# Performance work log

Measured on AMD Instinct MI355X. Metric: run time of the kernel, lower is better.

Reference implementation:

```python
import jax, jax.numpy as jnp
from jax import lax
import numpy as np

# (cin, cout, kernel, pad) for the 18 convs (funs 1,3,5,6,7,9,10,11,13..17,19..23)
CONVS = [(3,32,3,0),(32,64,3,0),(64,128,3,1),(128,64,1,0),(64,128,3,1),
         (128,256,3,1),(256,128,1,0),(128,256,3,0),(256,512,3,1),(512,256,1,0),
         (256,512,3,1),(512,256,1,0),(256,512,3,0),(512,256,3,1),(256,128,1,0),
         (128,64,3,1),(64,32,1,0),(32,6,3,1)]
# maxpool(2,2) after conv index (1-based) -> pool padding (torch pads with -inf, floor mode)
POOL_AFTER = {1: 1, 2: 1, 5: 0, 8: 1, 13: 1}
GT = (0.567, 0.469, 0.206, 0.53)  # hardcoded ground-truth box (cx, cy, w, h), normalized


def _backbone(x, ws, bs):
    for i, (w, b) in enumerate(zip(ws, bs), 1):
        pad = CONVS[i - 1][3]
        x = lax.conv_general_dilated(
            x, w, (1, 1), [(pad, pad), (pad, pad)],
            dimension_numbers=("NCHW", "OIHW", "NCHW")) + b[None, :, None, None]
        if i in POOL_AFTER:
            p = POOL_AFTER[i]
            x = lax.reduce_window(
                x, -jnp.inf, lax.max, (1, 1, 2, 2), (1, 1, 2, 2),
                [(0, 0), (0, 0), (p, p), (p, p)])
    return x


def _head(x):
    # torch: x.transpose(1,3) on [B,6,H,W] -> [B,W,H,6]; j indexes W, k indexes H
    xt = jnp.transpose(x, (0, 3, 2, 1))
    B, W, H, _ = xt.shape
    j = jnp.arange(W, dtype=xt.dtype)[None, :, None]  # [1,W,1]
    k = jnp.arange(H, dtype=xt.dtype)[None, None, :]  # [1,1,H]
    px = (j + xt[..., 2]) / W
    py = (k + xt[..., 3]) / H
    pw = jnp.exp(xt[..., 4]) / W
    ph = jnp.exp(xt[..., 5]) / H
    # center-format IoU against the single gt box (detached mask, as in torch via float())
    iw = jnp.clip(jnp.minimum(px + pw * 0.5, GT[0] + GT[2] * 0.5)
                  - jnp.maximum(px - pw * 0.5, GT[0] - GT[2] * 0.5), 0.0)
    ih = jnp.clip(jnp.minimum(py + ph * 0.5, GT[1] + GT[3] * 0.5)
                  - jnp.maximum(py - ph * 0.5, GT[1] - GT[3] * 0.5), 0.0)
    inter = iw * ih
    iou = inter / (pw * ph + GT[2] * GT[3] - inter)
    iou = lax.stop_gradient(iou)
    tx = GT[0] * W - j          # [1,W,1]
    ty = GT[1] * H - k          # [1,1,H]
    tw = np.log(GT[2] * W).astype(np.float32)
    th = np.log(GT[3] * H).astype(np.float32)
    l1 = (jnp.abs(tx - xt[..., 2]) + jnp.abs(ty - xt[..., 3])
          + jnp.abs(tw - xt[..., 4]) + jnp.abs(th - xt[..., 5]))
    loss = jnp.sum(jnp.where(iou > 0.5, l1, 0.0)).reshape(1)
    return xt, loss


def setup_inputs() -> dict:
    key = jax.random.key(0)
    keys = jax.random.split(key, 1 + 2 * len(CONVS))
    d = {"x": jax.random.normal(keys[0], (16, 3, 416, 416), jnp.float32)}
    for i, (cin, cout, ks, _) in enumerate(CONVS, 1):
        fan_in = cin * ks * ks
        d[f"w{i}"] = jax.random.normal(keys[2 * i - 1], (cout, cin, ks, ks), jnp.float32) / np.sqrt(fan_in)
        d[f"b{i}"] = jax.random.normal(keys[2 * i], (cout,), jnp.float32) * 0.01
    return d


def reference(x, w1, b1, w2, b2, w3, b3, w4, b4, w5, b5, w6, b6, w7, b7, w8, b8,
              w9, b9, w10, b10, w11, b11, w12, b12, w13, b13, w14, b14, w15, b15,
              w16, b16, w17, b17, w18, b18):
    ws = [w1, w2, w3, w4, w5, w6, w7, w8, w9, w10, w11, w12, w13, w14, w15, w16, w17, w18]
    bs = [b1, b2, b3, b4, b5, b6, b7, b8, b9, b10, b11, b12, b13, b14, b15, b16, b17, b18]
    feat = _backbone(x, ws, bs)
    xt, loss = _head(feat)
    return (xt, loss)
```

## Files before the change

### kernel.cpp

```cpp
#include <hip/hip_runtime.h>
#include <math.h>

typedef short v8s __attribute__((ext_vector_type(8)));
typedef float v4f __attribute__((ext_vector_type(4)));

template<int K, int COT, bool POOL, bool MASK, bool SWAP>
__global__ __launch_bounds__(256) void conv_fused(
    const float* __restrict__ in, const float* __restrict__ wgt,
    const float* __restrict__ bias, float* __restrict__ out,
    int B, int Cin, int Hin, int Win,
    int Hc, int Wc, int Hout, int Wout,
    int Cout, int cpad, int ppad,
    int inPS, int inRS, int inOfs, int outPS, int outRS, int outOfs)
{
    constexpr int NPY = POOL ? 2 : 1;
    constexpr int PS  = K + NPY - 1;
    const int spatial = Hout * Wout;
    const int idx = (SWAP ? blockIdx.y : blockIdx.x) * blockDim.x + threadIdx.x;
    const int cog = SWAP ? blockIdx.x : blockIdx.y;
    const int total = B * spatial;
    if (idx >= total) return;
    const int b  = idx / spatial;
    const int sp = idx - b * spatial;
    const int oy = sp / Wout;
    const int ox = sp - oy * Wout;
    const int co0 = cog * COT;

    const int cy0 = POOL ? (2 * oy - ppad) : oy;
    const int cx0 = POOL ? (2 * ox - ppad) : ox;
    const int iy0 = cy0 - cpad;
    const int ix0 = cx0 - cpad;

    bool my[PS], mx[PS];
#pragma unroll
    for (int i = 0; i < PS; i++) {
        my[i] = !MASK || ((unsigned)(iy0 + i) < (unsigned)Hin);
        mx[i] = !MASK || ((unsigned)(ix0 + i) < (unsigned)Win);
    }

    float acc[COT][NPY * NPY];
#pragma unroll
    for (int c = 0; c < COT; c++)
#pragma unroll
        for (int p = 0; p < NPY * NPY; p++) acc[c][p] = 0.f;

    const float* inB = in + inOfs + (size_t)b * Cin * inPS;
    const long wBase  = (long)co0 * Cin * K * K;

    for (int ci = 0; ci < Cin; ci++) {
        const float* ip = inB + (size_t)ci * inPS;
        float patch[PS][PS];
#pragma unroll
        for (int py = 0; py < PS; py++) {
#pragma unroll
            for (int px = 0; px < PS; px++) {
                float v = 0.f;
                if (my[py] && mx[px]) v = ip[(iy0 + py) * inRS + (ix0 + px)];
                patch[py][px] = v;
            }
        }
        const float* wp = wgt + wBase + (long)ci * K * K;
#pragma unroll
        for (int c = 0; c < COT; c++) {
#pragma unroll
            for (int kh = 0; kh < K; kh++)
#pragma unroll
            for (int kw = 0; kw < K; kw++) {
                const float wv = wp[(long)c * Cin * K * K + kh * K + kw];
#pragma unroll
                for (int dy = 0; dy < NPY; dy++)
#pragma unroll
                for (int dx = 0; dx < NPY; dx++)
                    acc[c][dy * NPY + dx] = fmaf(wv, patch[dy + kh][dx + kw],
                                                 acc[c][dy * NPY + dx]);
            }
        }
    }

#pragma unroll
    for (int c = 0; c < COT; c++) {
        float v;
        if (POOL) {
            v = -INFINITY;
#pragma unroll
            for (int dy = 0; dy < NPY; dy++)
#pragma unroll
            for (int dx = 0; dx < NPY; dx++) {
                const int cy = cy0 + dy, cx = cx0 + dx;
                if ((unsigned)cy < (unsigned)Hc && (unsigned)cx < (unsigned)Wc)
                    v = fmaxf(v, acc[c][dy * NPY + dx]);
            }
        } else {
            v = acc[c][0];
        }
        v += bias[co0 + c];
        out[outOfs + (size_t)(b * Cout + co0 + c) * outPS + oy * outRS + ox] = v;
    }
}

__global__ __launch_bounds__(256) void ring_zero(
    float* __restrict__ buf, int planes, int H, int W)
{
    int Wp = W + 2, Hp = H + 2;
    int ringlen = 2 * Wp + 2 * H;
    int t = blockIdx.x * 256 + threadIdx.x;
    if (t >= planes * ringlen) return;
    int p = t / ringlen, r = t - p * ringlen;
    float* pl = buf + (size_t)p * Hp * Wp;
    int idx;
    if (r < Wp) idx = r;
    else if (r < 2 * Wp) idx = (Hp - 1) * Wp + (r - Wp);
    else { int rr = r - 2 * Wp; int row = 1 + (rr >> 1); idx = row * Wp + ((rr & 1) ? (Wp - 1) : 0); }
    pl[idx] = 0.f;
}

__device__ __forceinline__ unsigned short f2bf_rne(float x) {
    unsigned u = __float_as_uint(x);
    return (unsigned short)((u + 0x7fffu + ((u >> 16) & 1u)) >> 16);
}
__device__ __forceinline__ float bf2f(unsigned short h) {
    return __uint_as_float(((unsigned)h) << 16);
}

__global__ __launch_bounds__(256) void prepack(
    const float* __restrict__ w, unsigned short* __restrict__ hi,
    unsigned short* __restrict__ lo, int cout, int kdim, int nkb)
{
    int t = blockIdx.x * 256 + threadIdx.x;
    if (t >= cout * kdim) return;
    int co = t / kdim, k = t - co * kdim;
    int cb = co >> 4, m = co & 15, kb = k >> 5, kk = k & 31;
    int lane = ((kk >> 3) << 4) | m, j = kk & 7;
    long dst = ((long)(cb * nkb + kb) << 9) + lane * 8 + j;
    float x = w[t];
    unsigned short h = f2bf_rne(x);
    hi[dst] = h;
    lo[dst] = f2bf_rne(x - bf2f(h));
}

template<int MT, int KS, bool SPLIT>
__global__ __launch_bounds__(256) void conv_mfma(
    const float* __restrict__ in, const unsigned short* __restrict__ whi,
    const unsigned short* __restrict__ wlo, const float* __restrict__ bias,
    float* __restrict__ out, int Cin, int inHWp, int inWp, int Hc, int Wc,
    int Cout, int pad, int b0, int nb, int nkbTot, int nkbPer, int Mpad,
    int outHWp, int outWp)
{
    const int HW = Hc * Wc;
    const int M = nb * HW;
    const int tid = threadIdx.x;
    const int lane = tid & 63;
    const int wv = tid >> 6;
    const int spBase = blockIdx.x * 64;
    const int kb0 = SPLIT ? blockIdx.z * nkbPer : 0;
    const int kb1 = SPLIT ? kb0 + nkbPer : nkbTot;

    __shared__ unsigned short P[2][5120];

    const int spoL = lane >> 2;
    int kkc[2];
    kkc[0] = (tid & 3) + 4 * wv;
    kkc[1] = kkc[0] + 16;

    const float* sptr[4];
    int soff[4];
#pragma unroll
    for (int j = 0; j < 4; ++j) {
        int sp = spBase + spoL + 16 * j;
        int q = sp < M ? sp : M - 1;
        int b = q / HW; int r = q - b * HW;
        int soy = r / Wc, sox = r - soy * Wc;
        soff[j] = (soy + 1) * inWp + (sox + 1);
        sptr[j] = in + (size_t)(b0 + b) * Cin * inHWp;
    }

    int ci[2], r9[2], koff[2];
#pragma unroll
    for (int m = 0; m < 2; ++m) {
        int k = kb0 * 32 + kkc[m];
        if (KS == 3) {
            ci[m] = k / 9; r9[m] = k - 9 * ci[m];
            int d3 = (r9[m] >= 3) + (r9[m] >= 6);
            koff[m] = ci[m] * inHWp + (d3 - pad) * inWp + (r9[m] - 3 * d3 - pad);
        } else { ci[m] = k; koff[m] = k * inHWp; }
    }

    float rv[8];
#define STAGE()                                                                \
    {                                                                          \
        _Pragma("unroll")                                                      \
        for (int m = 0; m < 2; ++m)                                            \
        _Pragma("unroll")                                                      \
        for (int j = 0; j < 4; ++j)                                            \
            rv[m * 4 + j] = sptr[j][koff[m] + soff[j]];                        \
    }
#define ADVANCE()                                                              \
    {                                                                          \
        _Pragma("unroll")                                                      \
        for (int m = 0; m < 2; ++m) {                                          \
            if (KS == 3) {                                                     \
                r9[m] += 5; int c = r9[m] >= 9; r9[m] -= c ? 9 : 0;            \
                ci[m] += 3 + c;                                                \
                int d3 = (r9[m] >= 3) + (r9[m] >= 6);                          \
                koff[m] = ci[m] * inHWp + (d3 - pad) * inWp                    \
                        + (r9[m] - 3 * d3 - pad);                              \
            } else { koff[m] += 32 * inHWp; }                                  \
        }                                                                      \
    }

    STAGE();

    const int g0 = blockIdx.y * (MT * 4) + wv * MT;
    const unsigned short* whp[MT];
    const unsigned short* wlp[MT];
#pragma unroll
    for (int mt = 0; mt < MT; ++mt) {
        size_t base = (((size_t)(g0 + mt) * nkbTot + kb0) << 9) + lane * 8;
        whp[mt] = whi + base; wlp[mt] = wlo + base;
    }

    v4f acc[MT][4];
    {
        v4f z = {0.f, 0.f, 0.f, 0.f};
#pragma unroll
        for (int mt = 0; mt < MT; ++mt)
#pragma unroll
            for (int nt = 0; nt < 4; ++nt) acc[mt][nt] = z;
    }

    for (int kb = kb0; kb < kb1; ++kb) {
        unsigned short* Ph = P[kb & 1];
#pragma unroll
        for (int m = 0; m < 2; ++m)
#pragma unroll
        for (int j = 0; j < 4; ++j) {
            float v = rv[m * 4 + j];
            unsigned vb = __float_as_uint(v);
            float res = v - __uint_as_float(vb & 0xffff0000u);
            int a = (spoL + 16 * j) * 40 + kkc[m];
            Ph[a] = (unsigned short)(vb >> 16);
            Ph[2560 + a] = (unsigned short)(__float_as_uint(res) >> 16);
        }
        __syncthreads();

        v8s wh[MT], wl[MT];
#pragma unroll
        for (int mt = 0; mt < MT; ++mt) {
            wh[mt] = *(const v8s*)whp[mt];
            wl[mt] = *(const v8s*)wlp[mt];
            whp[mt] += 512; wlp[mt] += 512;
        }

        if (kb + 1 < kb1) { ADVANCE(); STAGE(); }

#pragma unroll
        for (int nt = 0; nt < 4; ++nt) {
            int ro = (nt * 16 + (lane & 15)) * 40 + (lane >> 4) * 8;
            v8s ph = *(const v8s*)(Ph + ro);
            v8s pl = *(const v8s*)(Ph + 2560 + ro);
#pragma unroll
            for (int mt = 0; mt < MT; ++mt) {
                acc[mt][nt] = __builtin_amdgcn_mfma_f32_16x16x32_bf16(wh[mt], ph, acc[mt][nt], 0, 0, 0);
                acc[mt][nt] = __builtin_amdgcn_mfma_f32_16x16x32_bf16(wh[mt], pl, acc[mt][nt], 0, 0, 0);
                acc[mt][nt] = __builtin_amdgcn_mfma_f32_16x16x32_bf16(wl[mt], ph, acc[mt][nt], 0, 0, 0);
            }
        }
    }
#undef STAGE
#undef ADVANCE

    const int qrow = (lane >> 4) * 4;
    if (SPLIT) {
        float* pz = out + (size_t)blockIdx.z * Cout * Mpad;
#pragma unroll
        for (int mt = 0; mt < MT; ++mt) {
            int co = (g0 + mt) * 16 + qrow;
#pragma unroll
            for (int nt = 0; nt < 4; ++nt) {
                int sp = spBase + nt * 16 + (lane & 15);
                if (sp < M) {
#pragma unroll
                    for (int r = 0; r < 4; ++r)
                        pz[(size_t)(co + r) * Mpad + sp] = acc[mt][nt][r];
                }
            }
        }
    } else {
#pragma unroll
        for (int mt = 0; mt < MT; ++mt) {
            int co = (g0 + mt) * 16 + qrow;
            float bsv[4];
#pragma unroll
            for (int r = 0; r < 4; ++r) bsv[r] = bias[co + r];
#pragma unroll
            for (int nt = 0; nt < 4; ++nt) {
                int sp = spBase + nt * 16 + (lane & 15);
                if (sp < M) {
                    int b = sp / HW, rsp = sp - b * HW;
                    int y = rsp / Wc, xx = rsp - y * Wc;
                    float* op = out + (size_t)(b * Cout + co) * outHWp
                              + (size_t)(y + 1) * outWp + (xx + 1);
#pragma unroll
                    for (int r = 0; r < 4; ++r)
                        op[(size_t)r * outHWp] = acc[mt][nt][r] + bsv[r];
                }
            }
        }
    }
}

__global__ __launch_bounds__(256) void sk_reduce(
    const float* __restrict__ part, const float* __restrict__ bias,
    float* __restrict__ out, int Cout, int HW, int Wc, int M, int Mpad, int SK,
    int outHWp, int outWp)
{
    int t = blockIdx.x * 256 + threadIdx.x;
    if (t >= Cout * M) return;
    int co = t / M, m = t - co * M;
    float s = bias[co];
    for (int k = 0; k < SK; ++k)
        s += part[((size_t)k * Cout + co) * Mpad + m];
    int b = m / HW, rsp = m - b * HW;
    int y = rsp / Wc, xx = rsp - y * Wc;
    out[(size_t)(b * Cout + co) * outHWp + (size_t)(y + 1) * outWp + (xx + 1)] = s;
}

__global__ __launch_bounds__(256) void maxpool_k(
    const float* __restrict__ in, float* __restrict__ out,
    int Hc, int Wc, int Hp, int Wp, int p, int total,
    int inHWp, int inWp, int outHWp, int outWp)
{
    int t = blockIdx.x * 256 + threadIdx.x;
    if (t >= total) return;
    int wp2 = Hp * Wp;
    int bc = t / wp2; int r = t - bc * wp2;
    int y = r / Wp, xx = r - y * Wp;
    int y0 = 2 * y - p, x0 = 2 * xx - p;
    const float* ip = in + (size_t)bc * inHWp;
    float v = -INFINITY;
#pragma unroll
    for (int dy = 0; dy < 2; ++dy)
#pragma unroll
    for (int dx = 0; dx < 2; ++dx) {
        int yy = y0 + dy, xc = x0 + dx;
        if ((unsigned)yy < (unsigned)Hc && (unsigned)xc < (unsigned)Wc)
            v = fmaxf(v, ip[(yy + 1) * inWp + (xc + 1)]);
    }
    out[(size_t)bc * outHWp + (size_t)(y + 1) * outWp + (xx + 1)] = v;
}

__global__ __launch_bounds__(1024) void head_kernel(
    const float* __restrict__ x, float* __restrict__ out, int B)
{
    const int W = 13, H = 13;
    const float gx = 0.567f, gy = 0.469f, gw = 0.206f, gh = 0.53f;
    const int tid = threadIdx.x;
    const int total = B * W * H;
    float lsum = 0.f;
    for (int i = tid; i < total; i += blockDim.x) {
        const int b = i / (W * H);
        const int r = i - b * W * H;
        const int j = r / H;
        const int k = r - j * H;
        float v[6];
#pragma unroll
        for (int c = 0; c < 6; c++) {
            v[c] = x[((b * 6 + c) * H + k) * W + j];
            out[((b * W + j) * H + k) * 6 + c] = v[c];
        }
        const float px = (j + v[2]) / (float)W;
        const float py = (k + v[3]) / (float)H;
        const float pw = expf(v[4]) / (float)W;
        const float ph = expf(v[5]) / (float)H;
        float iw = fminf(px + pw * 0.5f, gx + gw * 0.5f)
                 - fmaxf(px - pw * 0.5f, gx - gw * 0.5f);
        iw = fmaxf(iw, 0.f);
        float ih = fminf(py + ph * 0.5f, gy + gh * 0.5f)
                 - fmaxf(py - ph * 0.5f, gy - gh * 0.5f);
        ih = fmaxf(ih, 0.f);
        const float inter = iw * ih;
        const float iou = inter / (pw * ph + gw * gh - inter);
        const float tx = gx * W - (float)j;
        const float ty = gy * H - (float)k;
        const float tw = logf(gw * W);
        const float th = logf(gh * H);
        const float l1 = fabsf(tx - v[2]) + fabsf(ty - v[3])
                       + fabsf(tw - v[4]) + fabsf(th - v[5]);
        if (iou > 0.5f) lsum += l1;
    }
    __shared__ float red[1024];
    red[tid] = lsum;
    __syncthreads();
    for (int s = blockDim.x / 2; s > 0; s >>= 1) {
        if (tid < s) red[tid] += red[tid + s];
        __syncthreads();
    }
    if (tid == 0) out[total * 6] = red[0];
}

extern "C" void kernel_launch(void* const* d_in, const int* in_sizes, int n_in,
                              void* d_out, int out_size, void* d_ws, size_t ws_size,
                              hipStream_t stream)
{
    (void)in_sizes; (void)n_in; (void)out_size;
    const float* x = (const float*)d_in[0];
    const int B = 16;
    const size_t MB = 1024 * 1024;
    char* ws = (char*)d_ws;
    float* bufA = (float*)ws;
    float* bufB = (float*)(ws + 93 * MB);
    unsigned short* WHI = (unsigned short*)(ws + 141 * MB);
    unsigned short* WLO = (unsigned short*)(ws + 153 * MB);
    char* TEMP = ws + 165 * MB;
    const bool gemmOK = ws_size >= 166 * MB;
    const size_t tempAvail = ws_size > 165 * MB ? ws_size - 165 * MB : 0;

    static const struct { int cin, cout, ks, cpad, pool, ppad; } L[18] = {
        {3,  32, 3, 0, 1, 1}, {32, 64, 3, 0, 1, 1}, {64, 128, 3, 1, 0, 0},
        {128, 64, 1, 0, 0, 0}, {64, 128, 3, 1, 1, 0}, {128, 256, 3, 1, 0, 0},
        {256, 128, 1, 0, 0, 0}, {128, 256, 3, 0, 1, 1}, {256, 512, 3, 1, 0, 0},
        {512, 256, 1, 0, 0, 0}, {256, 512, 3, 1, 0, 0}, {512, 256, 1, 0, 0, 0},
        {256, 512, 3, 0, 1, 1}, {512, 256, 3, 1, 0, 0}, {256, 128, 1, 0, 0, 0},
        {128, 64, 3, 1, 0, 0}, {64, 32, 1, 0, 0, 0}, {32, 6, 3, 1, 0, 0}
    };
    static const bool RING[18] = {0,1,0,1,1,0,0,1,0,1,0,0,1,0,1,0,1,0};

    if (gemmOK) {
        size_t off = 0;
        for (int i = 1; i <= 15; ++i) {
            int kdim = L[i].cin * L[i].ks * L[i].ks;
            int n = L[i].cout * kdim;
            prepack<<<(n + 255) / 256, 256, 0, stream>>>(
                (const float*)d_in[2 * i + 1], WHI + off, WLO + off,
                L[i].cout, kdim, kdim / 32);
            off += (size_t)n;
        }
    }

    const float* cur = x;
    int Hin = 416, Win = 416;
    size_t woff = 0;

    for (int i = 0; i < 18; ++i) {
        const auto& l = L[i];
        const int Hc = Hin + 2 * l.cpad - l.ks + 1;
        const int Wc = Win + 2 * l.cpad - l.ks + 1;
        const int Hout = l.pool ? (Hc + 2 * l.ppad - 2) / 2 + 1 : Hc;
        const int Wout = l.pool ? (Wc + 2 * l.ppad - 2) / 2 + 1 : Wc;
        float* dst = (i % 2 == 0) ? bufA : bufB;
        const float* w  = (const float*)d_in[2 * i + 1];
        const float* bb = (const float*)d_in[2 * i + 2];
        const int kdim = l.cin * l.ks * l.ks;
        const int nkb = kdim / 32;

        const int inRS  = (i == 0) ? Win : (Win + 2);
        const int inPS  = (i == 0) ? Hin * Win : (Hin + 2) * (Win + 2);
        const int inOfs = (i == 0) ? 0 : (inRS + 1);
        const bool outPad = (i != 17);
        const int outRS  = outPad ? (Wout + 2) : Wout;
        const int outPS  = outPad ? (Hout + 2) * (Wout + 2) : Hout * Wout;
        const int outOfs = outPad ? (outRS + 1) : 0;
        const int tRS = Wc + 2, tPS = (Hc + 2) * (Wc + 2);

        if (RING[i]) {
            int planes = B * l.cout;
            int ringlen = 2 * (Wout + 2) + 2 * Hout;
            ring_zero<<<(planes * ringlen + 255) / 256, 256, 0, stream>>>(
                dst, planes, Hout, Wout);
        }

        int nb = 16;
        if (l.pool) {
            size_t perImg = (size_t)l.cout * tPS * 4;
            while (nb && perImg * (size_t)nb > tempAvail) nb >>= 1;
        }
        const bool useG = gemmOK && i >= 1 && i <= 15 && (!l.pool || nb >= 1);

        if (useG) {
            for (int b0 = 0; b0 < B; b0 += nb) {
                const int M = nb * Hc * Wc;
                const int gx = (M + 63) / 64;
                int MTv = (l.cout >= 256 && (long)gx * (l.cout / 256) >= 512) ? 4
                        : (l.cout >= 128 && (long)gx * (l.cout / 128) >= 512) ? 2 : 1;
                int gy = l.cout / (MTv * 64);
                int SK = 1;
                if (!l.pool && (long)gx * gy < 512) {
                    if (nkb % 4 == 0 && (size_t)4 * l.cout * gx * 64 * 4 <= tempAvail) SK = 4;
                    else if (nkb % 2 == 0 && (size_t)2 * l.cout * gx * 64 * 4 <= tempAvail) SK = 2;
                }
                const int nkbPer = nkb / SK;
                const int Mpad = gx * 64;
                float* gout = l.pool ? (float*)TEMP : (SK > 1 ? (float*)TEMP : dst);
                const int gHWp = l.pool ? tPS : (SK > 1 ? 0 : outPS);
                const int gWp  = l.pool ? tRS : (SK > 1 ? 0 : outRS);
                dim3 gr(gx, gy, SK);
#define GL(MTC, KSC, SPL)                                                      \
                conv_mfma<MTC, KSC, SPL><<<gr, 256, 0, stream>>>(              \
                    cur, WHI + woff, WLO + woff, bb, gout, l.cin, inPS, inRS,  \
                    Hc, Wc, l.cout, l.cpad, b0, nb, nkb, nkbPer, Mpad,         \
                    gHWp, gWp)
#define G2(MTC, KSC) do { if (SK > 1) GL(MTC, KSC, true); else GL(MTC, KSC, false); } while (0)
                if (MTv == 4)      { if (l.ks == 3) G2(4, 3); else G2(4, 1); }
                else if (MTv == 2) { if (l.ks == 3) G2(2, 3); else G2(2, 1); }
                else               { if (l.ks == 3) G2(1, 3); else G2(1, 1); }
#undef G2
#undef GL
                if (SK > 1) {
                    int tot = l.cout * M;
                    sk_reduce<<<(tot + 255) / 256, 256, 0, stream>>>(
                        (const float*)TEMP, bb, dst, l.cout, Hc * Wc, Wc, M,
                        Mpad, SK, outPS, outRS);
                }
                if (l.pool) {
                    int total = nb * l.cout * Hout * Wout;
                    maxpool_k<<<(total + 255) / 256, 256, 0, stream>>>(
                        (const float*)TEMP,
                        dst + (size_t)b0 * l.cout * outPS,
                        Hc, Wc, Hout, Wout, l.ppad, total, tPS, tRS, outPS, outRS);
                }
            }
        } else {
            const int spatial = Hout * Wout;
#define FL(KK, CC, PP, MM, SW)                                                 \
            conv_fused<KK, CC, PP, MM, SW><<<                                  \
                SW ? dim3(l.cout / CC, (B * spatial + 255) / 256)              \
                   : dim3((B * spatial + 255) / 256, l.cout / CC),             \
                256, 0, stream>>>(                                             \
                cur, w, bb, dst, B, l.cin, Hin, Win, Hc, Wc, Hout, Wout,       \
                l.cout, l.cpad, l.ppad, inPS, inRS, inOfs, outPS, outRS, outOfs)
            if (i == 0)                           FL(3, 8, true, true, true);
            else if (i == 16)                     FL(1, 8, false, false, false);
            else if (i == 17)                     FL(3, 6, false, false, false);
            else if (l.pool)                      FL(3, 4, true, true, false);
            else if (l.ks == 3)                   FL(3, 8, false, true, false);
            else                                  FL(1, 8, false, true, false);
#undef FL
        }

        if (i >= 1 && i <= 15) woff += (size_t)l.cout * kdim;
        cur = dst;
        Hin = Hout;
        Win = Wout;
    }

    head_kernel<<<1, 1024, 0, stream>>>(cur, (float*)d_out, B);
}
```

Baseline: 1.520 ms.

## Switch activations to padded NHWC and vectorize MFMA conv staging, add 128-wide tile kernel

Moves intermediate activations from padded NCHW planes to a padded NHWC (channel-last) layout. The MFMA implicit-GEMM kernel can then load four consecutive input channels as one v4f and pack bf16 hi/lo pairs into LDS with vector stores. It also adds a double-buffered register prefetch, a 128-row spatial tile variant for layers with 128 or fewer output channels, and a revised split-K/MT selection heuristic. The goal is to cut scattered scalar global loads and LDS stores in the GEMM staging and raise occupancy and reuse. The cost is rewritten ring-zero, prepack, maxpool and reduce indexing, plus more register pressure.

```diff
diff --git a/kernel.cpp b/kernel.cpp
--- a/kernel.cpp
+++ b/kernel.cpp
@@ -3,6 +3,7 @@
 
 typedef short v8s __attribute__((ext_vector_type(8)));
 typedef float v4f __attribute__((ext_vector_type(4)));
+typedef unsigned uu2 __attribute__((ext_vector_type(2)));
 
 template<int K, int COT, bool POOL, bool MASK, bool SWAP>
 __global__ __launch_bounds__(256) void conv_fused(
@@ -11,7 +12,8 @@
     int B, int Cin, int Hin, int Win,
     int Hc, int Wc, int Hout, int Wout,
     int Cout, int cpad, int ppad,
-    int inPS, int inRS, int inOfs, int outPS, int outRS, int outOfs)
+    long inBS, long inCS, int inRS, int inXS, long inOfs,
+    long outBS, long outCS, int outRS, int outXS, long outOfs)
 {
     constexpr int NPY = POOL ? 2 : 1;
     constexpr int PS  = K + NPY - 1;
@@ -44,18 +46,19 @@
 #pragma unroll
         for (int p = 0; p < NPY * NPY; p++) acc[c][p] = 0.f;
 
-    const float* inB = in + inOfs + (size_t)b * Cin * inPS;
-    const long wBase  = (long)co0 * Cin * K * K;
+    const float* inB = in + inOfs + (size_t)b * inBS;
+    const long wBase = (long)co0 * Cin * K * K;
 
     for (int ci = 0; ci < Cin; ci++) {
-        const float* ip = inB + (size_t)ci * inPS;
+        const float* ip = inB + (size_t)ci * inCS;
         float patch[PS][PS];
 #pragma unroll
         for (int py = 0; py < PS; py++) {
 #pragma unroll
             for (int px = 0; px < PS; px++) {
                 float v = 0.f;
-                if (my[py] && mx[px]) v = ip[(iy0 + py) * inRS + (ix0 + px)];
+                if (my[py] && mx[px])
+                    v = ip[(iy0 + py) * inRS + (ix0 + px) * inXS];
                 patch[py][px] = v;
             }
         }
@@ -94,24 +97,33 @@
             v = acc[c][0];
         }
         v += bias[co0 + c];
-        out[outOfs + (size_t)(b * Cout + co0 + c) * outPS + oy * outRS + ox] = v;
+        out[outOfs + (size_t)b * outBS + (size_t)(co0 + c) * outCS
+            + oy * outRS + ox * outXS] = v;
     }
 }
 
 __global__ __launch_bounds__(256) void ring_zero(
-    float* __restrict__ buf, int planes, int H, int W)
+    float* __restrict__ buf, int B, int H, int W, int C4)
 {
     int Wp = W + 2, Hp = H + 2;
-    int ringlen = 2 * Wp + 2 * H;
+    int rl4 = (2 * Wp + 2 * H) * C4;
     int t = blockIdx.x * 256 + threadIdx.x;
-    if (t >= planes * ringlen) return;
-    int p = t / ringlen, r = t - p * ringlen;
-    float* pl = buf + (size_t)p * Hp * Wp;
-    int idx;
-    if (r < Wp) idx = r;
-    else if (r < 2 * Wp) idx = (Hp - 1) * Wp + (r - Wp);
-    else { int rr = r - 2 * Wp; int row = 1 + (rr >> 1); idx = row * Wp + ((rr & 1) ? (Wp - 1) : 0); }
-    pl[idx] = 0.f;
+    if (t >= B * rl4) return;
+    int p = t / rl4, r = t - p * rl4;
+    int top = Wp * C4;
+    int idx4;
+    if (r < top) idx4 = r;
+    else if (r < 2 * top) idx4 = (Hp - 1) * Wp * C4 + (r - top);
+    else {
+        r -= 2 * top;
+        int row = 1 + r / (2 * C4);
+        int rr = r - (row - 1) * (2 * C4);
+        int side = rr / C4;
+        int cc = rr - side * C4;
+        idx4 = (row * Wp + side * (Wp - 1)) * C4 + cc;
+    }
+    v4f z = {0.f, 0.f, 0.f, 0.f};
+    ((v4f*)buf)[(size_t)p * Hp * Wp * C4 + idx4] = z;
 }
 
 __device__ __forceinline__ unsigned short f2bf_rne(float x) {
@@ -124,11 +136,14 @@
 
 __global__ __launch_bounds__(256) void prepack(
     const float* __restrict__ w, unsigned short* __restrict__ hi,
-    unsigned short* __restrict__ lo, int cout, int kdim, int nkb)
-{
+    unsigned short* __restrict__ lo, int cout, int cin, int ksq, int nkb)
+{
+    int kdim = cin * ksq;
     int t = blockIdx.x * 256 + threadIdx.x;
     if (t >= cout * kdim) return;
-    int co = t / kdim, k = t - co * kdim;
+    int co = t / kdim, rem = t - co * kdim;
+    int ci = rem / ksq, off = rem - ci * ksq;
+    int k = off * cin + ci;
     int cb = co >> 4, m = co & 15, kb = k >> 5, kk = k & 31;
     int lane = ((kk >> 3) << 4) | m, j = kk & 7;
     long dst = ((long)(cb * nkb + kb) << 9) + lane * 8 + j;
@@ -138,13 +153,31 @@
     lo[dst] = f2bf_rne(x - bf2f(h));
 }
 
+#define PACK_LDSW(PL, V, ROW, KQ)                                              \
+    {                                                                          \
+        unsigned a0 = __float_as_uint((V)[0]), a1 = __float_as_uint((V)[1]);   \
+        unsigned a2 = __float_as_uint((V)[2]), a3 = __float_as_uint((V)[3]);   \
+        float r0 = (V)[0] - __uint_as_float(a0 & 0xffff0000u);                 \
+        float r1 = (V)[1] - __uint_as_float(a1 & 0xffff0000u);                 \
+        float r2 = (V)[2] - __uint_as_float(a2 & 0xffff0000u);                 \
+        float r3 = (V)[3] - __uint_as_float(a3 & 0xffff0000u);                 \
+        uu2 hp, lp;                                                            \
+        hp[0] = (a0 >> 16) | (a1 & 0xffff0000u);                               \
+        hp[1] = (a2 >> 16) | (a3 & 0xffff0000u);                               \
+        lp[0] = (__float_as_uint(r0) >> 16) | (__float_as_uint(r1) & 0xffff0000u); \
+        lp[1] = (__float_as_uint(r2) >> 16) | (__float_as_uint(r3) & 0xffff0000u); \
+        int a_ = (ROW) * 40 + 4 * (KQ);                                        \
+        *(uu2*)((PL) + a_) = hp;                                               \
+        *(uu2*)((PL) + (LOHALF) + a_) = lp;                                    \
+    }
+
 template<int MT, int KS, bool SPLIT>
 __global__ __launch_bounds__(256) void conv_mfma(
     const float* __restrict__ in, const unsigned short* __restrict__ whi,
     const unsigned short* __restrict__ wlo, const float* __restrict__ bias,
-    float* __restrict__ out, int Cin, int inHWp, int inWp, int Hc, int Wc,
-    int Cout, int pad, int b0, int nb, int nkbTot, int nkbPer, int Mpad,
-    int outHWp, int outWp)
+    float* __restrict__ out, int Cin, int inBS, int inRow, int Hc, int Wc,
+    int Cout, int pad, int b0, int nb, int nkbTot, int nkbPer,
+    int Mpad, int outBS, int outRow)
 {
     const int HW = Hc * Wc;
     const int M = nb * HW;
@@ -153,62 +186,51 @@
     const int wv = tid >> 6;
     const int spBase = blockIdx.x * 64;
     const int kb0 = SPLIT ? blockIdx.z * nkbPer : 0;
-    const int kb1 = SPLIT ? kb0 + nkbPer : nkbTot;
-
+    const int n = SPLIT ? nkbPer : nkbTot;
+
+#define LOHALF 2560
     __shared__ unsigned short P[2][5120];
 
-    const int spoL = lane >> 2;
-    int kkc[2];
-    kkc[0] = (tid & 3) + 4 * wv;
-    kkc[1] = kkc[0] + 16;
-
-    const float* sptr[4];
-    int soff[4];
-#pragma unroll
-    for (int j = 0; j < 4; ++j) {
-        int sp = spBase + spoL + 16 * j;
+    const int spo = tid >> 3;
+    const int kq  = tid & 7;
+
+    int jbase[2];
+#pragma unroll
+    for (int j = 0; j < 2; ++j) {
+        int sp = spBase + spo + 32 * j;
         int q = sp < M ? sp : M - 1;
         int b = q / HW; int r = q - b * HW;
-        int soy = r / Wc, sox = r - soy * Wc;
-        soff[j] = (soy + 1) * inWp + (sox + 1);
-        sptr[j] = in + (size_t)(b0 + b) * Cin * inHWp;
-    }
-
-    int ci[2], r9[2], koff[2];
-#pragma unroll
-    for (int m = 0; m < 2; ++m) {
-        int k = kb0 * 32 + kkc[m];
+        int y = r / Wc, x = r - y * Wc;
+        jbase[j] = (b0 + b) * inBS + (y + 1) * inRow + (x + 1) * Cin;
+    }
+
+    int koff, rowrem = 0, rowChunks = 0;
+    {
+        int k0 = kb0 * 32;
         if (KS == 3) {
-            ci[m] = k / 9; r9[m] = k - 9 * ci[m];
-            int d3 = (r9[m] >= 3) + (r9[m] >= 6);
-            koff[m] = ci[m] * inHWp + (d3 - pad) * inWp + (r9[m] - 3 * d3 - pad);
-        } else { ci[m] = k; koff[m] = k * inHWp; }
-    }
-
-    float rv[8];
-#define STAGE()                                                                \
+            int off0 = k0 / Cin;
+            int ci0 = k0 - off0 * Cin;
+            int dy0 = off0 / 3, dx0 = off0 - 3 * dy0;
+            int cinCh = Cin >> 5;
+            rowChunks = 3 * cinCh;
+            rowrem = rowChunks - (dx0 * cinCh + (ci0 >> 5));
+            koff = (dy0 - pad) * inRow + (dx0 - pad) * Cin + ci0 + 4 * kq;
+        } else {
+            koff = k0 + 4 * kq;
+        }
+    }
+
+#define STAGE(F)                                                               \
     {                                                                          \
-        _Pragma("unroll")                                                      \
-        for (int m = 0; m < 2; ++m)                                            \
-        _Pragma("unroll")                                                      \
-        for (int j = 0; j < 4; ++j)                                            \
-            rv[m * 4 + j] = sptr[j][koff[m] + soff[j]];                        \
-    }
-#define ADVANCE()                                                              \
+        F[0] = *(const v4f*)(in + jbase[0] + koff);                            \
+        F[1] = *(const v4f*)(in + jbase[1] + koff);                            \
+    }
+#define ADV()                                                                  \
     {                                                                          \
-        _Pragma("unroll")                                                      \
-        for (int m = 0; m < 2; ++m) {                                          \
-            if (KS == 3) {                                                     \
-                r9[m] += 5; int c = r9[m] >= 9; r9[m] -= c ? 9 : 0;            \
-                ci[m] += 3 + c;                                                \
-                int d3 = (r9[m] >= 3) + (r9[m] >= 6);                          \
-                koff[m] = ci[m] * inHWp + (d3 - pad) * inWp                    \
-                        + (r9[m] - 3 * d3 - pad);                              \
-            } else { koff[m] += 32 * inHWp; }                                  \
-        }                                                                      \
-    }
-
-    STAGE();
+        if (KS == 3 && --rowrem == 0) {                                        \
+            rowrem = rowChunks; koff += inRow - 3 * Cin + 32;                  \
+        } else koff += 32;                                                     \
+    }
 
     const int g0 = blockIdx.y * (MT * 4) + wv * MT;
     const unsigned short* whp[MT];
@@ -228,36 +250,175 @@
             for (int nt = 0; nt < 4; ++nt) acc[mt][nt] = z;
     }
 
-    for (int kb = kb0; kb < kb1; ++kb) {
-        unsigned short* Ph = P[kb & 1];
-#pragma unroll
-        for (int m = 0; m < 2; ++m)
-#pragma unroll
-        for (int j = 0; j < 4; ++j) {
-            float v = rv[m * 4 + j];
-            unsigned vb = __float_as_uint(v);
-            float res = v - __uint_as_float(vb & 0xffff0000u);
-            int a = (spoL + 16 * j) * 40 + kkc[m];
-            Ph[a] = (unsigned short)(vb >> 16);
-            Ph[2560 + a] = (unsigned short)(__float_as_uint(res) >> 16);
-        }
+    v4f rv0[2], rv1[2];
+    STAGE(rv0); ADV();
+    if (n > 1) { STAGE(rv1); }
+    ADV();
+
+#define BODY(RV)                                                               \
+    {                                                                          \
+        unsigned short* Pl = &P[cc & 1][0];                                    \
+        PACK_LDSW(Pl, RV[0], spo, kq);                                         \
+        PACK_LDSW(Pl, RV[1], spo + 32, kq);                                    \
+        __syncthreads();                                                       \
+        v8s wh[MT], wl[MT];                                                    \
+        _Pragma("unroll")                                                      \
+        for (int mt = 0; mt < MT; ++mt) {                                      \
+            wh[mt] = *(const v8s*)whp[mt]; whp[mt] += 512;                     \
+            wl[mt] = *(const v8s*)wlp[mt]; wlp[mt] += 512;                     \
+        }                                                                      \
+        if (cc + 2 < n) { STAGE(RV); ADV(); }                                  \
+        _Pragma("unroll")                                                      \
+        for (int nt = 0; nt < 4; ++nt) {                                       \
+            int ro = (nt * 16 + (lane & 15)) * 40 + (lane >> 4) * 8;           \
+            v8s ph = *(const v8s*)(Pl + ro);                                   \
+            v8s pl = *(const v8s*)(Pl + LOHALF + ro);                          \
+            _Pragma("unroll")                                                  \
+            for (int mt = 0; mt < MT; ++mt) {                                  \
+                acc[mt][nt] = __builtin_amdgcn_mfma_f32_16x16x32_bf16(         \
+                    wh[mt], ph, acc[mt][nt], 0, 0, 0);                         \
+                acc[mt][nt] = __builtin_amdgcn_mfma_f32_16x16x32_bf16(         \
+                    wh[mt], pl, acc[mt][nt], 0, 0, 0);                         \
+                acc[mt][nt] = __builtin_amdgcn_mfma_f32_16x16x32_bf16(         \
+                    wl[mt], ph, acc[mt][nt], 0, 0, 0);                         \
+            }                                                                  \
+        }                                                                      \
+    }
+
+    int cc = 0;
+    for (;;) {
+        BODY(rv0);
+        if (++cc >= n) break;
+        BODY(rv1);
+        if (++cc >= n) break;
+    }
+#undef BODY
+#undef STAGE
+#undef ADV
+#undef LOHALF
+
+    const int qrow = (lane >> 4) * 4;
+    if (SPLIT) {
+        float* pz = out + (size_t)blockIdx.z * Mpad * Cout;
+#pragma unroll
+        for (int mt = 0; mt < MT; ++mt) {
+            int co = (g0 + mt) * 16 + qrow;
+#pragma unroll
+            for (int nt = 0; nt < 4; ++nt) {
+                int sp = spBase + nt * 16 + (lane & 15);
+                if (sp < M)
+                    *(v4f*)(pz + (size_t)sp * Cout + co) = acc[mt][nt];
+            }
+        }
+    } else {
+#pragma unroll
+        for (int mt = 0; mt < MT; ++mt) {
+            int co = (g0 + mt) * 16 + qrow;
+            v4f bs = *(const v4f*)(bias + co);
+#pragma unroll
+            for (int nt = 0; nt < 4; ++nt) {
+                int sp = spBase + nt * 16 + (lane & 15);
+                if (sp < M) {
+                    int b = sp / HW, rsp = sp - b * HW;
+                    int y = rsp / Wc, x = rsp - y * Wc;
+                    v4f o = acc[mt][nt] + bs;
+                    *(v4f*)(out + (size_t)b * outBS + (y + 1) * outRow
+                            + (x + 1) * Cout + co) = o;
+                }
+            }
+        }
+    }
+}
+
+template<int MT, int KS>
+__global__ __launch_bounds__(256) void conv_mfma_n128(
+    const float* __restrict__ in, const unsigned short* __restrict__ whi,
+    const unsigned short* __restrict__ wlo, const float* __restrict__ bias,
+    float* __restrict__ out, int Cin, int inBS, int inRow, int Hc, int Wc,
+    int Cout, int pad, int b0, int nb, int nkbTot, int outBS, int outRow)
+{
+    const int HW = Hc * Wc;
+    const int M = nb * HW;
+    const int tid = threadIdx.x;
+    const int lane = tid & 63;
+    const int wv = tid >> 6;
+    const int spBase = blockIdx.x * 128;
+
+#define LOHALF 5120
+    __shared__ unsigned short P[10240];
+
+    const int spo = tid >> 3;
+    const int kq  = tid & 7;
+
+    int jbase[4];
+#pragma unroll
+    for (int j = 0; j < 4; ++j) {
+        int sp = spBase + spo + 32 * j;
+        int q = sp < M ? sp : M - 1;
+        int b = q / HW; int r = q - b * HW;
+        int y = r / Wc, x = r - y * Wc;
+        jbase[j] = (b0 + b) * inBS + (y + 1) * inRow + (x + 1) * Cin;
+    }
+
+    int koff, rowrem = 0, rowChunks = 0;
+    if (KS == 3) {
+        int cinCh = Cin >> 5;
+        rowChunks = 3 * cinCh;
+        rowrem = rowChunks;
+        koff = (0 - pad) * inRow + (0 - pad) * Cin + 4 * kq;
+    } else {
+        koff = 4 * kq;
+    }
+
+    v4f rv[4];
+#pragma unroll
+    for (int j = 0; j < 4; ++j) rv[j] = *(const v4f*)(in + jbase[j] + koff);
+
+    const int g0 = blockIdx.y * (MT * 4) + wv * MT;
+    const unsigned short* whp[MT];
+    const unsigned short* wlp[MT];
+#pragma unroll
+    for (int mt = 0; mt < MT; ++mt) {
+        size_t base = ((size_t)(g0 + mt) * nkbTot << 9) + lane * 8;
+        whp[mt] = whi + base; wlp[mt] = wlo + base;
+    }
+
+    v4f acc[MT][8];
+    {
+        v4f z = {0.f, 0.f, 0.f, 0.f};
+#pragma unroll
+        for (int mt = 0; mt < MT; ++mt)
+#pragma unroll
+            for (int nt = 0; nt < 8; ++nt) acc[mt][nt] = z;
+    }
+
+    for (int cc = 0; cc < nkbTot; ++cc) {
+#pragma unroll
+        for (int j = 0; j < 4; ++j)
+            PACK_LDSW(P, rv[j], spo + 32 * j, kq);
         __syncthreads();
 
         v8s wh[MT], wl[MT];
 #pragma unroll
         for (int mt = 0; mt < MT; ++mt) {
-            wh[mt] = *(const v8s*)whp[mt];
-            wl[mt] = *(const v8s*)wlp[mt];
-            whp[mt] += 512; wlp[mt] += 512;
-        }
-
-        if (kb + 1 < kb1) { ADVANCE(); STAGE(); }
-
-#pragma unroll
-        for (int nt = 0; nt < 4; ++nt) {
+            wh[mt] = *(const v8s*)whp[mt]; whp[mt] += 512;
+            wl[mt] = *(const v8s*)wlp[mt]; wlp[mt] += 512;
+        }
+
+        if (cc + 1 < nkbTot) {
+            if (KS == 3 && --rowrem == 0) {
+                rowrem = rowChunks; koff += inRow - 3 * Cin + 32;
+            } else koff += 32;
+#pragma unroll
+            for (int j = 0; j < 4; ++j)
+                rv[j] = *(const v4f*)(in + jbase[j] + koff);
+        }
+
+#pragma unroll
+        for (int nt = 0; nt < 8; ++nt) {
             int ro = (nt * 16 + (lane & 15)) * 40 + (lane >> 4) * 8;
-            v8s ph = *(const v8s*)(Ph + ro);
-            v8s pl = *(const v8s*)(Ph + 2560 + ro);
+            v8s ph = *(const v8s*)(P + ro);
+            v8s pl = *(const v8s*)(P + LOHALF + ro);
 #pragma unroll
             for (int mt = 0; mt < MT; ++mt) {
                 acc[mt][nt] = __builtin_amdgcn_mfma_f32_16x16x32_bf16(wh[mt], ph, acc[mt][nt], 0, 0, 0);
@@ -265,45 +426,24 @@
                 acc[mt][nt] = __builtin_amdgcn_mfma_f32_16x16x32_bf16(wl[mt], ph, acc[mt][nt], 0, 0, 0);
             }
         }
-    }
-#undef STAGE
-#undef ADVANCE
+        __syncthreads();
+    }
+#undef LOHALF
 
     const int qrow = (lane >> 4) * 4;
-    if (SPLIT) {
-        float* pz = out + (size_t)blockIdx.z * Cout * Mpad;
-#pragma unroll
-        for (int mt = 0; mt < MT; ++mt) {
-            int co = (g0 + mt) * 16 + qrow;
-#pragma unroll
-            for (int nt = 0; nt < 4; ++nt) {
-                int sp = spBase + nt * 16 + (lane & 15);
-                if (sp < M) {
-#pragma unroll
-                    for (int r = 0; r < 4; ++r)
-                        pz[(size_t)(co + r) * Mpad + sp] = acc[mt][nt][r];
-                }
-            }
-        }
-    } else {
-#pragma unroll
-        for (int mt = 0; mt < MT; ++mt) {
-            int co = (g0 + mt) * 16 + qrow;
-            float bsv[4];
-#pragma unroll
-            for (int r = 0; r < 4; ++r) bsv[r] = bias[co + r];
-#pragma unroll
-            for (int nt = 0; nt < 4; ++nt) {
-                int sp = spBase + nt * 16 + (lane & 15);
-                if (sp < M) {
-                    int b = sp / HW, rsp = sp - b * HW;
-                    int y = rsp / Wc, xx = rsp - y * Wc;
-                    float* op = out + (size_t)(b * Cout + co) * outHWp
-                              + (size_t)(y + 1) * outWp + (xx + 1);
-#pragma unroll
-                    for (int r = 0; r < 4; ++r)
-                        op[(size_t)r * outHWp] = acc[mt][nt][r] + bsv[r];
-                }
+#pragma unroll
+    for (int mt = 0; mt < MT; ++mt) {
+        int co = (g0 + mt) * 16 + qrow;
+        v4f bs = *(const v4f*)(bias + co);
+#pragma unroll
+        for (int nt = 0; nt < 8; ++nt) {
+            int sp = spBase + nt * 16 + (lane & 15);
+            if (sp < M) {
+                int b = sp / HW, rsp = sp - b * HW;
+                int y = rsp / Wc, x = rsp - y * Wc;
+                v4f o = acc[mt][nt] + bs;
+                *(v4f*)(out + (size_t)b * outBS + (y + 1) * outRow
+                        + (x + 1) * Cout + co) = o;
             }
         }
     }
@@ -312,41 +452,48 @@
 __global__ __launch_bounds__(256) void sk_reduce(
     const float* __restrict__ part, const float* __restrict__ bias,
     float* __restrict__ out, int Cout, int HW, int Wc, int M, int Mpad, int SK,
-    int outHWp, int outWp)
-{
+    int outBS, int outRow)
+{
+    int C4 = Cout >> 2;
     int t = blockIdx.x * 256 + threadIdx.x;
-    if (t >= Cout * M) return;
-    int co = t / M, m = t - co * M;
-    float s = bias[co];
+    if (t >= M * C4) return;
+    int m = t / C4, cq = t - m * C4;
+    int co = 4 * cq;
+    v4f s = *(const v4f*)(bias + co);
     for (int k = 0; k < SK; ++k)
-        s += part[((size_t)k * Cout + co) * Mpad + m];
+        s += *(const v4f*)(part + ((size_t)k * Mpad + m) * Cout + co);
     int b = m / HW, rsp = m - b * HW;
-    int y = rsp / Wc, xx = rsp - y * Wc;
-    out[(size_t)(b * Cout + co) * outHWp + (size_t)(y + 1) * outWp + (xx + 1)] = s;
+    int y = rsp / Wc, x = rsp - y * Wc;
+    *(v4f*)(out + (size_t)b * outBS + (y + 1) * outRow + (x + 1) * Cout + co) = s;
 }
 
 __global__ __launch_bounds__(256) void maxpool_k(
     const float* __restrict__ in, float* __restrict__ out,
-    int Hc, int Wc, int Hp, int Wp, int p, int total,
-    int inHWp, int inWp, int outHWp, int outWp)
-{
+    int Hc, int Wc, int Hp, int Wp, int p, int total4, int C,
+    int inBS, int inRow, int outBS, int outRow, int b0)
+{
+    int C4 = C >> 2;
     int t = blockIdx.x * 256 + threadIdx.x;
-    if (t >= total) return;
-    int wp2 = Hp * Wp;
-    int bc = t / wp2; int r = t - bc * wp2;
-    int y = r / Wp, xx = r - y * Wp;
-    int y0 = 2 * y - p, x0 = 2 * xx - p;
-    const float* ip = in + (size_t)bc * inHWp;
-    float v = -INFINITY;
+    if (t >= total4) return;
+    int cq = t % C4; int rest = t / C4;
+    int x = rest % Wp; rest /= Wp;
+    int y = rest % Hp; int bl = rest / Hp;
+    int y0 = 2 * y - p, x0 = 2 * x - p;
+    v4f v = {-INFINITY, -INFINITY, -INFINITY, -INFINITY};
 #pragma unroll
     for (int dy = 0; dy < 2; ++dy)
 #pragma unroll
     for (int dx = 0; dx < 2; ++dx) {
         int yy = y0 + dy, xc = x0 + dx;
-        if ((unsigned)yy < (unsigned)Hc && (unsigned)xc < (unsigned)Wc)
-            v = fmaxf(v, ip[(yy + 1) * inWp + (xc + 1)]);
-    }
-    out[(size_t)bc * outHWp + (size_t)(y + 1) * outWp + (xx + 1)] = v;
+        if ((unsigned)yy < (unsigned)Hc && (unsigned)xc < (unsigned)Wc) {
+            v4f u = *(const v4f*)(in + (size_t)bl * inBS + (yy + 1) * inRow
+                                  + (xc + 1) * C + 4 * cq);
+            v[0] = fmaxf(v[0], u[0]); v[1] = fmaxf(v[1], u[1]);
+            v[2] = fmaxf(v[2], u[2]); v[3] = fmaxf(v[3], u[3]);
+        }
+    }
+    *(v4f*)(out + (size_t)(b0 + bl) * outBS + (y + 1) * outRow
+            + (x + 1) * C + 4 * cq) = v;
 }
 
 __global__ __launch_bounds__(1024) void head_kernel(
@@ -413,7 +560,7 @@
     unsigned short* WLO = (unsigned short*)(ws + 153 * MB);
     char* TEMP = ws + 165 * MB;
     const bool gemmOK = ws_size >= 166 * MB;
-    const size_t tempAvail = ws_size > 165 * MB ? ws_size - 165 * MB : 0;
+    const size_t tempAvail = ws_size > 166 * MB ? ws_size - 166 * MB : 0;
 
     static const struct { int cin, cout, ks, cpad, pool, ppad; } L[18] = {
         {3,  32, 3, 0, 1, 1}, {32, 64, 3, 0, 1, 1}, {64, 128, 3, 1, 0, 0},
@@ -432,7 +579,7 @@
             int n = L[i].cout * kdim;
             prepack<<<(n + 255) / 256, 256, 0, stream>>>(
                 (const float*)d_in[2 * i + 1], WHI + off, WLO + off,
-                L[i].cout, kdim, kdim / 32);
+                L[i].cout, L[i].cin, L[i].ks * L[i].ks, kdim / 32);
             off += (size_t)n;
         }
     }
@@ -453,85 +600,116 @@
         const int kdim = l.cin * l.ks * l.ks;
         const int nkb = kdim / 32;
 
-        const int inRS  = (i == 0) ? Win : (Win + 2);
-        const int inPS  = (i == 0) ? Hin * Win : (Hin + 2) * (Win + 2);
-        const int inOfs = (i == 0) ? 0 : (inRS + 1);
-        const bool outPad = (i != 17);
-        const int outRS  = outPad ? (Wout + 2) : Wout;
-        const int outPS  = outPad ? (Hout + 2) * (Wout + 2) : Hout * Wout;
-        const int outOfs = outPad ? (outRS + 1) : 0;
-        const int tRS = Wc + 2, tPS = (Hc + 2) * (Wc + 2);
+        const int inRow = (Win + 2) * l.cin;
+        const int inBS  = (Hin + 2) * inRow;
+        const int outRow = (Wout + 2) * l.cout;
+        const int outBS  = (Hout + 2) * outRow;
+        const int tRow = (Wc + 2) * l.cout;
+        const int tBS  = (Hc + 2) * tRow;
 
         if (RING[i]) {
-            int planes = B * l.cout;
-            int ringlen = 2 * (Wout + 2) + 2 * Hout;
-            ring_zero<<<(planes * ringlen + 255) / 256, 256, 0, stream>>>(
-                dst, planes, Hout, Wout);
+            int rl4 = (2 * (Wout + 2) + 2 * Hout) * (l.cout / 4);
+            ring_zero<<<(B * rl4 + 255) / 256, 256, 0, stream>>>(
+                dst, B, Hout, Wout, l.cout / 4);
         }
 
         int nb = 16;
-        if (l.pool) {
-            size_t perImg = (size_t)l.cout * tPS * 4;
-            while (nb && perImg * (size_t)nb > tempAvail) nb >>= 1;
+        if (l.pool && i >= 1) {
+            size_t perImg = (size_t)tBS * 4;
+            while (nb > 1 && perImg * (size_t)nb + MB > tempAvail) nb >>= 1;
+            if (perImg + MB > tempAvail) nb = 0;
         }
         const bool useG = gemmOK && i >= 1 && i <= 15 && (!l.pool || nb >= 1);
 
         if (useG) {
             for (int b0 = 0; b0 < B; b0 += nb) {
                 const int M = nb * Hc * Wc;
-                const int gx = (M + 63) / 64;
-                int MTv = (l.cout >= 256 && (long)gx * (l.cout / 256) >= 512) ? 4
-                        : (l.cout >= 128 && (long)gx * (l.cout / 128) >= 512) ? 2 : 1;
-                int gy = l.cout / (MTv * 64);
-                int SK = 1;
-                if (!l.pool && (long)gx * gy < 512) {
-                    if (nkb % 4 == 0 && (size_t)4 * l.cout * gx * 64 * 4 <= tempAvail) SK = 4;
-                    else if (nkb % 2 == 0 && (size_t)2 * l.cout * gx * 64 * 4 <= tempAvail) SK = 2;
-                }
-                const int nkbPer = nkb / SK;
-                const int Mpad = gx * 64;
-                float* gout = l.pool ? (float*)TEMP : (SK > 1 ? (float*)TEMP : dst);
-                const int gHWp = l.pool ? tPS : (SK > 1 ? 0 : outPS);
-                const int gWp  = l.pool ? tRS : (SK > 1 ? 0 : outRS);
-                dim3 gr(gx, gy, SK);
+                float* gout = l.pool ? (float*)TEMP : dst;
+                const int gBS  = l.pool ? tBS : outBS;
+                const int gRow = l.pool ? tRow : outRow;
+                const int gx128 = (M + 127) / 128;
+                const bool n128 = (l.cout <= 128) && (gx128 >= 512);
+
+                if (n128) {
+                    const int MTn = (l.cout >= 128) ? 2 : 1;
+                    dim3 gr(gx128, l.cout / (MTn * 64));
+#define NL(MTC, KSC)                                                           \
+                    conv_mfma_n128<MTC, KSC><<<gr, 256, 0, stream>>>(          \
+                        cur, WHI + woff, WLO + woff, bb, gout, l.cin, inBS,    \
+                        inRow, Hc, Wc, l.cout, l.cpad, b0, nb, nkb, gBS, gRow)
+                    if (MTn == 2) { if (l.ks == 3) NL(2, 3); else NL(2, 1); }
+                    else          { if (l.ks == 3) NL(1, 3); else NL(1, 1); }
+#undef NL
+                } else {
+                    const int gx = (M + 63) / 64;
+                    const int Mpad = gx * 64;
+                    int MTv = (l.cout >= 256) ? 4 : (l.cout >= 128 ? 2 : 1);
+                    int gy = l.cout / (MTv * 64);
+                    while (MTv > 1 && (long)gx * gy < 512) {
+                        MTv >>= 1; gy = l.cout / (MTv * 64);
+                    }
+                    int SK = 1;
+                    if (!l.pool && (long)gx * gy < 512) {
+                        MTv = (l.cout >= 256) ? 4 : (l.cout >= 128 ? 2 : 1);
+                        gy = l.cout / (MTv * 64);
+                        while ((long)gx * gy * SK < 512 && SK < 16 &&
+                               nkb % (SK * 2) == 0 &&
+                               (size_t)(SK * 2) * Mpad * l.cout * 4 + MB <= tempAvail)
+                            SK *= 2;
+                    }
+                    const int nkbPer = nkb / SK;
+                    float* kout = (SK > 1) ? (float*)TEMP : gout;
+                    dim3 gr(gx, gy, SK);
 #define GL(MTC, KSC, SPL)                                                      \
-                conv_mfma<MTC, KSC, SPL><<<gr, 256, 0, stream>>>(              \
-                    cur, WHI + woff, WLO + woff, bb, gout, l.cin, inPS, inRS,  \
-                    Hc, Wc, l.cout, l.cpad, b0, nb, nkb, nkbPer, Mpad,         \
-                    gHWp, gWp)
+                    conv_mfma<MTC, KSC, SPL><<<gr, 256, 0, stream>>>(          \
+                        cur, WHI + woff, WLO + woff, bb, kout, l.cin, inBS,    \
+                        inRow, Hc, Wc, l.cout, l.cpad, b0, nb, nkb, nkbPer,    \
+                        Mpad, gBS, gRow)
 #define G2(MTC, KSC) do { if (SK > 1) GL(MTC, KSC, true); else GL(MTC, KSC, false); } while (0)
-                if (MTv == 4)      { if (l.ks == 3) G2(4, 3); else G2(4, 1); }
-                else if (MTv == 2) { if (l.ks == 3) G2(2, 3); else G2(2, 1); }
-                else               { if (l.ks == 3) G2(1, 3); else G2(1, 1); }
+                    if (MTv == 4)      { if (l.ks == 3) G2(4, 3); else G2(4, 1); }
+                    else if (MTv == 2) { if (l.ks == 3) G2(2, 3); else G2(2, 1); }
+                    else               { if (l.ks == 3) G2(1, 3); else G2(1, 1); }
 #undef G2
 #undef GL
-                if (SK > 1) {
-                    int tot = l.cout * M;
-                    sk_reduce<<<(tot + 255) / 256, 256, 0, stream>>>(
-                        (const float*)TEMP, bb, dst, l.cout, Hc * Wc, Wc, M,
-                        Mpad, SK, outPS, outRS);
+                    if (SK > 1) {
+                        int tot4 = M * (l.cout / 4);
+                        sk_reduce<<<(tot4 + 255) / 256, 256, 0, stream>>>(
+                            (const float*)TEMP, bb, dst, l.cout, Hc * Wc, Wc,
+                            M, Mpad, SK, outBS, outRow);
+                    }
                 }
                 if (l.pool) {
-                    int total = nb * l.cout * Hout * Wout;
-                    maxpool_k<<<(total + 255) / 256, 256, 0, stream>>>(
-                        (const float*)TEMP,
-                        dst + (size_t)b0 * l.cout * outPS,
-                        Hc, Wc, Hout, Wout, l.ppad, total, tPS, tRS, outPS, outRS);
+                    int total4 = nb * (Hout + 2) * (Wout + 2) * (l.cout / 4);
+                    total4 = nb * Hout * Wout * (l.cout / 4);
+                    maxpool_k<<<(total4 + 255) / 256, 256, 0, stream>>>(
+                        (const float*)TEMP, dst, Hc, Wc, Hout, Wout, l.ppad,
+                        total4, l.cout, tBS, tRow, outBS, outRow, b0);
                 }
             }
         } else {
             const int spatial = Hout * Wout;
+            long iBS, iCS, iOfs; int iRS, iXS;
+            if (i == 0) { iBS = (long)l.cin * Hin * Win; iCS = (long)Hin * Win;
+                          iRS = Win; iXS = 1; iOfs = 0; }
+            else        { iBS = inBS; iCS = 1; iRS = inRow; iXS = l.cin;
+                          iOfs = (long)inRow + l.cin; }
+            long oBS, oCS, oOfs; int oRS, oXS;
+            if (i == 17) { oBS = (long)l.cout * spatial; oCS = spatial;
+                           oRS = Wout; oXS = 1; oOfs = 0; }
+            else         { oBS = outBS; oCS = 1; oRS = outRow; oXS = l.cout;
+                           oOfs = (long)outRow + l.cout; }
 #define FL(KK, CC, PP, MM, SW)                                                 \
             conv_fused<KK, CC, PP, MM, SW><<<                                  \
                 SW ? dim3(l.cout / CC, (B * spatial + 255) / 256)              \
                    : dim3((B * spatial + 255) / 256, l.cout / CC),             \
                 256, 0, stream>>>(                                             \
                 cur, w, bb, dst, B, l.cin, Hin, Win, Hc, Wc, Hout, Wout,       \
-                l.cout, l.cpad, l.ppad, inPS, inRS, inOfs, outPS, outRS, outOfs)
+                l.cout, l.cpad, l.ppad,                                        \
+                iBS, iCS, iRS, iXS, iOfs, oBS, oCS, oRS, oXS, oOfs)
             if (i == 0)                           FL(3, 8, true, true, true);
             else if (i == 16)                     FL(1, 8, false, false, false);
             else if (i == 17)                     FL(3, 6, false, false, false);
-            else if (l.pool)                      FL(3, 4, true, true, false);
+            else if (l.pool)                      FL(3, 8, true, true, false);
             else if (l.ks == 3)                   FL(3, 8, false, true, false);
             else                                  FL(1, 8, false, true, false);
 #undef FL
```

After: 1.478 ms. 2.7% less time.
